# Kernel tuning notes

Hardware: AMD Instinct MI355X
Metric: run time of the kernel (lower is better)

Reference implementation:

```python
import jax, jax.numpy as jnp
import numpy as np

N = 3000          # num_sample (nodes)
N_OMICS = 3000    # input feature dims for both omics
ENC1, ENC2, NZ = 256, 128, 64


def _xavier(key, fan_in, fan_out):
    limit = float(np.sqrt(6.0 / (fan_in + fan_out)))
    return jax.random.uniform(key, (fan_in, fan_out), jnp.float32, -limit, limit)


def setup_inputs() -> dict:
    key = jax.random.key(0)
    ks = jax.random.split(key, 20)
    inp = {
        "omics_1": jax.random.normal(ks[0], (N, N_OMICS), jnp.float32),
        "omics_2": jax.random.normal(ks[1], (N, N_OMICS), jnp.float32),
    }
    # random dense adjacency, row-normalized (as a typical normalized graph operator)
    for i, name in enumerate(["adj_feature_omics1", "adj_feature_omics2",
                              "adj_spatial_omics1", "adj_spatial_omics2"]):
        a = jax.random.uniform(ks[2 + i], (N, N), jnp.float32)
        inp[name] = a / jnp.sum(a, axis=1, keepdims=True)
    # GNNLayer weights for the four GAE encoders (xavier uniform, as in reset_parameters)
    dims = [(N_OMICS, ENC1), (ENC1, ENC2), (ENC2, NZ)]
    kidx = 6
    for enc in ["f1", "f2", "s1", "s2"]:
        for li, (fi, fo) in enumerate(dims, start=1):
            inp[f"w_{enc}_{li}"] = _xavier(ks[kidx], fi, fo)
            kidx += 1
    return inp


def _gae_encoder(x, adj, w1, w2, w3):
    # GNNLayer: support = act(x @ W); out = spmm(adj, support). Dropout is identity (eval).
    z = adj @ jnp.tanh(x @ w1)          # [N, ENC1]
    z = adj @ jnp.tanh(z @ w2)          # [N, ENC2]
    z = adj @ (z @ w3)                  # [N, NZ]  (no activation on layer 3)
    adj_hat = jax.nn.sigmoid(z @ z.T)   # [N, N]
    return z, adj_hat


def reference(omics_1, omics_2,
              adj_feature_omics1, adj_feature_omics2,
              adj_spatial_omics1, adj_spatial_omics2,
              w_f1_1, w_f1_2, w_f1_3,
              w_f2_1, w_f2_2, w_f2_3,
              w_s1_1, w_s1_2, w_s1_3,
              w_s2_1, w_s2_2, w_s2_3):
    _, a1 = _gae_encoder(omics_1, adj_feature_omics1, w_f1_1, w_f1_2, w_f1_3)
    _, a2 = _gae_encoder(omics_2, adj_feature_omics2, w_f2_1, w_f2_2, w_f2_3)
    _, a3 = _gae_encoder(omics_1, adj_spatial_omics1, w_s1_1, w_s1_2, w_s1_3)
    _, a4 = _gae_encoder(omics_2, adj_spatial_omics2, w_s2_1, w_s2_2, w_s2_3)
    # stacked reconstructed adjacencies from the four encoders [4, N, N]
    return jnp.stack([a1, a2, a3, a4], axis=0)
```

## Files before the change

### kernel.cpp

```cpp
#include <hip/hip_runtime.h>
#include <stdint.h>
#include <stddef.h>


typedef __attribute__((ext_vector_type(8))) _Float16 half8;
typedef __attribute__((ext_vector_type(4))) float f32x4;

#define PAD 3072
#define MR  3000
#define SQ_STRIDE ((size_t)PAD * PAD)
#define UPA (PAD * PAD / 8)
#define CAST_BLK 576
#define WT_BLK   128

static __device__ __forceinline__ void async_cp16(const _Float16* g, _Float16* l) {
    __builtin_amdgcn_global_load_lds((const __attribute__((address_space(1))) void*)g,
                                     (__attribute__((address_space(3))) void*)l, 16, 0, 0);
}

struct PrepArgs {
    const float* csrc[2];  _Float16* cdst[2];
    const float* Wsrc[12]; _Float16* Wdst[3];
};

__global__ __launch_bounds__(256) void prep2(PrepArgs p) {
    __shared__ _Float16 lt[64 * 64];
    const int b = blockIdx.x;
    const int t = threadIdx.x;
    if (b < CAST_BLK) {
        const int TOT = 2 * UPA;
        for (int base = b * 2048; base < TOT; base += CAST_BLK * 2048) {
            f32x4 v[8][2];
            #pragma unroll
            for (int k = 0; k < 8; ++k) {
                const int u   = base + (k << 8) + t;
                const int arr = u / UPA;
                const int rem = u - arr * UPA;
                const int row = rem / 384;
                const int c0  = (rem - row * 384) * 8;
                if (row < MR && c0 < MR) {
                    const float* sp = p.csrc[arr] + (size_t)row * MR + c0;
                    v[k][0] = __builtin_nontemporal_load((const f32x4*)sp);
                    v[k][1] = __builtin_nontemporal_load((const f32x4*)(sp + 4));
                } else {
                    v[k][0] = (f32x4){0.f, 0.f, 0.f, 0.f};
                    v[k][1] = (f32x4){0.f, 0.f, 0.f, 0.f};
                }
            }
            #pragma unroll
            for (int k = 0; k < 8; ++k) {
                const int u   = base + (k << 8) + t;
                const int arr = u / UPA;
                const int rem = u - arr * UPA;
                const int row = rem / 384;
                const int c0  = (rem - row * 384) * 8;
                half8 h;
                #pragma unroll
                for (int j = 0; j < 4; ++j) {
                    h[j]     = (_Float16)v[k][0][j];
                    h[4 + j] = (_Float16)v[k][1][j];
                }
                *(half8*)(p.cdst[arr] + (size_t)row * PAD + c0) = h;
            }
        }
    } else {
        for (int tile = b - CAST_BLK; tile < 816; tile += WT_BLK) {
            const int enc = tile / 204;
            int rem = tile - enc * 204;
            const float* src; _Float16* dst; int fi, fo, ldk, kt, rt;
            if (rem < 192) {
                src = p.Wsrc[enc * 3 + 0]; dst = p.Wdst[0] + (size_t)enc * 256 * PAD;
                fi = MR; fo = 256; ldk = PAD; kt = rem >> 2; rt = rem & 3;
            } else if (rem < 200) {
                rem -= 192;
                src = p.Wsrc[enc * 3 + 1]; dst = p.Wdst[1] + (size_t)enc * 128 * 256;
                fi = 256; fo = 128; ldk = 256; kt = rem >> 1; rt = rem & 1;
            } else {
                rem -= 200;
                src = p.Wsrc[enc * 3 + 2]; dst = p.Wdst[2] + (size_t)enc * 128 * 128;
                fi = 128; fo = 64; ldk = 128; kt = rem >> 1; rt = rem & 1;
            }
            const int k0 = kt * 64, r0 = rt * 64;
            __syncthreads();
            {
                const int kr = t >> 2, cc = (t & 3) << 4;
                const int gk = k0 + kr;
                const bool kok = gk < fi;
                #pragma unroll
                for (int j = 0; j < 16; ++j) {
                    const int gr = r0 + cc + j;
                    const float v = (kok && gr < fo) ? src[(size_t)gk * fo + gr] : 0.f;
                    lt[(cc + j) * 64 + kr] = (_Float16)v;
                }
            }
            __syncthreads();
            {
                const int rr = t >> 2, kk = (t & 3) << 4;
                half8 a  = *(half8*)&lt[rr * 64 + kk];
                half8 bb = *(half8*)&lt[rr * 64 + kk + 8];
                _Float16* dp = dst + (size_t)(r0 + rr) * ldk + k0 + kk;
                *(half8*)dp = a;
                *(half8*)(dp + 8) = bb;
            }
        }
    }
}

struct GArgs {
    const _Float16* Aall; size_t aStride; int aMask;
    const _Float16* Ball; size_t bStride; int bMask;
    void* Call; size_t cStride;
    int M, Ncols, Kp, lda, ldb, ldc, mBound, nBound;
};
struct CastA { const float* src[4]; _Float16* dst; };

template<int ACT, int OMODE, int S, int CAST>
__global__ __launch_bounds__(256, 3)
void gemm_bt(GArgs ga, CastA ca)
{
    __shared__ _Float16 smem[16384];

    const int z   = blockIdx.z;
    const int e   = z / S;
    const int ksl = z - e * S;
    const int Kslice = ga.Kp / S;
    const int kbase  = ksl * Kslice;

    const _Float16* A = ga.Aall + (size_t)(e & ga.aMask) * ga.aStride;
    const _Float16* B = ga.Ball + (size_t)(e & ga.bMask) * ga.bStride;

    const int tm = blockIdx.x * 128;
    const int tn = blockIdx.y * 128;
    const int t    = threadIdx.x;
    const int lane = t & 63;
    const int w    = t >> 6;
    const int wm   = (w >> 1) * 64;
    const int wn   = (w & 1) * 64;
    const int lr   = lane & 15;
    const int lg   = lane >> 4;

    const int sr  = t >> 2;
    const int sch = t & 3;

    f32x4 acc[4][4];
    const f32x4 zero = {0.f, 0.f, 0.f, 0.f};
    #pragma unroll
    for (int i = 0; i < 4; ++i)
        #pragma unroll
        for (int j = 0; j < 4; ++j) acc[i][j] = zero;

    const int nht = Kslice >> 5;

    const int fid = blockIdx.x + gridDim.x * (blockIdx.y + gridDim.y * blockIdx.z);
    f32x4 cv0, cv1;
    _Float16* cdp = nullptr;

    auto STAGE = [&](int ht, int buf) {
        const int k0 = kbase + (ht << 5);
        _Float16* As = smem + buf * 8192;
        _Float16* Bs = As + 4096;
        #pragma unroll
        for (int i = 0; i < 2; ++i) {
            const int row = sr + i * 64;
            const int sc  = sch ^ (row & 3);
            async_cp16(A + (size_t)(tm + row) * ga.lda + k0 + sc * 8,
                       As + (row * 4 + sch) * 8);
        }
        #pragma unroll
        for (int i = 0; i < 2; ++i) {
            const int row = sr + i * 64;
            const int sc  = sch ^ (row & 3);
            async_cp16(B + (size_t)(tn + row) * ga.ldb + k0 + sc * 8,
                       Bs + (row * 4 + sch) * 8);
        }
    };

    STAGE(0, 0);
    __syncthreads();
    for (int h = 0; h < nht; ++h) {
        const int cur = h & 1;
        if (h + 1 < nht) STAGE(h + 1, cur ^ 1);
        if (CAST) {
            if (h > 0) {
                half8 hh;
                #pragma unroll
                for (int j = 0; j < 4; ++j) {
                    hh[j] = (_Float16)cv0[j]; hh[4 + j] = (_Float16)cv1[j];
                }
                *(half8*)cdp = hh;
            }
            const int g    = (fid * nht + h) * 256 + t;
            const int arr  = g / UPA;
            const int rem  = g - arr * UPA;
            const int crow = rem / 384;
            const int cc0  = (rem - crow * 384) * 8;
            cdp = ca.dst + (size_t)arr * SQ_STRIDE + (size_t)crow * PAD + cc0;
            if (crow < MR && cc0 < MR) {
                const float* sp = ca.src[arr] + (size_t)crow * MR + cc0;
                cv0 = __builtin_nontemporal_load((const f32x4*)sp);
                cv1 = __builtin_nontemporal_load((const f32x4*)(sp + 4));
            } else {
                cv0 = (f32x4){0.f, 0.f, 0.f, 0.f};
                cv1 = (f32x4){0.f, 0.f, 0.f, 0.f};
            }
        }
        const _Float16* As = smem + cur * 8192;
        const _Float16* Bs = As + 4096;
        half8 af[4], bf[4];
        #pragma unroll
        for (int mi = 0; mi < 4; ++mi) {
            const int ra = wm + mi * 16 + lr;
            const int ch = lg ^ (ra & 3);
            af[mi] = *(const half8*)(As + ra * 32 + ch * 8);
        }
        #pragma unroll
        for (int ni = 0; ni < 4; ++ni) {
            const int rb = wn + ni * 16 + lr;
            const int ch = lg ^ (rb & 3);
            bf[ni] = *(const half8*)(Bs + rb * 32 + ch * 8);
        }
        #pragma unroll
        for (int mi = 0; mi < 4; ++mi)
            #pragma unroll
            for (int ni = 0; ni < 4; ++ni)
                acc[mi][ni] = __builtin_amdgcn_mfma_f32_16x16x32_f16(
                    af[mi], bf[ni], acc[mi][ni], 0, 0, 0);
        __syncthreads();
    }
    if (CAST) {
        half8 hh;
        #pragma unroll
        for (int j = 0; j < 4; ++j) {
            hh[j] = (_Float16)cv0[j]; hh[4 + j] = (_Float16)cv1[j];
        }
        *(half8*)cdp = hh;
    }

    if (OMODE == 0) {
        _Float16* C = (_Float16*)ga.Call + (size_t)e * ga.cStride;
        #pragma unroll
        for (int mi = 0; mi < 4; ++mi)
            #pragma unroll
            for (int rr = 0; rr < 4; ++rr) {
                const int m = tm + wm + mi * 16 + lg * 4 + rr;
                #pragma unroll
                for (int ni = 0; ni < 4; ++ni) {
                    const int n = tn + wn + ni * 16 + lr;
                    float x = acc[mi][ni][rr];
                    if (ACT) x = tanhf(x);
                    const bool ok = (m < ga.M) && (n < ga.Ncols);
                    C[(size_t)m * ga.ldc + n] = ok ? (_Float16)x : (_Float16)0.f;
                }
            }
    } else if (OMODE == 1) {
        _Float16* Cp = (_Float16*)ga.Call + (size_t)z * ga.cStride;
        _Float16* ep = smem + w * 2048;
        #pragma unroll
        for (int hs = 0; hs < 2; ++hs) {
            __syncthreads();
            #pragma unroll
            for (int mi2 = 0; mi2 < 2; ++mi2)
                #pragma unroll
                for (int ni = 0; ni < 4; ++ni)
                    #pragma unroll
                    for (int rr = 0; rr < 4; ++rr) {
                        const int row = mi2 * 16 + lg * 4 + rr;
                        const int col = ni * 16 + lr;
                        const int sw  = (((row ^ (row >> 2)) & 3) << 4);
                        ep[row * 64 + (col ^ sw)] = (_Float16)acc[hs * 2 + mi2][ni][rr];
                    }
            __syncthreads();
            #pragma unroll
            for (int it = 0; it < 4; ++it) {
                const int row = it * 8 + (lane >> 3);
                const int c0  = (lane & 7) * 8;
                const int sw  = (((row ^ (row >> 2)) & 3) << 4);
                half8 v = *(const half8*)&ep[row * 64 + (c0 ^ sw)];
                const int gm = tm + wm + hs * 32 + row;
                const int gn = tn + wn + c0;
                *(half8*)&((_Float16*)Cp)[(size_t)gm * ga.ldc + gn] = v;
            }
        }
    } else {
        float* Cp = (float*)ga.Call + (size_t)e * ga.cStride;
        float* ep = (float*)smem + w * 2048;
        #pragma unroll
        for (int hs = 0; hs < 2; ++hs) {
            __syncthreads();
            #pragma unroll
            for (int mi2 = 0; mi2 < 2; ++mi2)
                #pragma unroll
                for (int ni = 0; ni < 4; ++ni)
                    #pragma unroll
                    for (int rr = 0; rr < 4; ++rr) {
                        const int row = mi2 * 16 + lg * 4 + rr;
                        const int col = ni * 16 + lr;
                        const int sw  = (((row ^ (row >> 2)) & 3) << 4);
                        ep[row * 64 + (col ^ sw)] = acc[hs * 2 + mi2][ni][rr];
                    }
            __syncthreads();
            #pragma unroll
            for (int r2 = 0; r2 < 8; ++r2) {
                const int row = r2 * 4 + (lane >> 4);
                const int c4  = (lane & 15) * 4;
                const int sw  = (((row ^ (row >> 2)) & 3) << 4);
                f32x4 v = *(const f32x4*)&ep[row * 64 + (c4 ^ sw)];
                const int gm = tm + wm + hs * 32 + row;
                const int gn = tn + wn + c4;
                if (gm < ga.mBound && gn < ga.nBound) {
                    #pragma unroll
                    for (int j = 0; j < 4; ++j)
                        v[j] = 1.0f / (1.0f + __expf(-v[j]));
                    __builtin_nontemporal_store(v, (f32x4*)&Cp[(size_t)gm * ga.ldc + gn]);
                }
            }
        }
    }
}

template<int ACT, int S>
__global__ __launch_bounds__(256)
void reduce_k(const _Float16* __restrict__ P, _Float16* __restrict__ out, size_t region)
{
    const size_t e    = blockIdx.y;
    const size_t base = (size_t)(blockIdx.x * 256 + threadIdx.x) * 8;
    const _Float16* p0 = P + e * S * region + base;
    float s[8] = {0.f, 0.f, 0.f, 0.f, 0.f, 0.f, 0.f, 0.f};
    #pragma unroll
    for (int si = 0; si < S; ++si) {
        half8 v = *(const half8*)(p0 + (size_t)si * region);
        #pragma unroll
        for (int j = 0; j < 8; ++j) s[j] += (float)v[j];
    }
    half8 h;
    #pragma unroll
    for (int j = 0; j < 8; ++j) {
        float x = s[j];
        if (ACT) x = tanhf(x);
        h[j] = (_Float16)x;
    }
    *(half8*)(out + e * region + base) = h;
}

extern "C" void kernel_launch(void* const* d_in, const int* in_sizes, int n_in,
                              void* d_out, int out_size, void* d_ws, size_t ws_size,
                              hipStream_t stream)
{
    const size_t R1 = 786432;
    const size_t R2 = 393216;

    _Float16* Adj    = (_Float16*)d_out;
    _Float16* Part16 = Adj + 4 * SQ_STRIDE;

    _Float16* hb = (_Float16*)d_ws;
    size_t off = 0;
    auto alloc = [&](size_t elems) { _Float16* p = hb + off; off += elems; return p; };
    _Float16* Xh  = alloc(2 * SQ_STRIDE);
    _Float16* T1  = alloc(4 * R1);
    _Float16* Z1  = alloc(4 * R1);
    _Float16* T2  = alloc(4 * R2);
    _Float16* Z2  = alloc(4 * R2);
    _Float16* T3  = alloc(4 * R2);
    _Float16* Z3  = alloc(4 * R2);
    _Float16* W1t = alloc(4ull * 256 * PAD);
    _Float16* W2t = alloc(4ull * 128 * 256);
    _Float16* W3t = alloc(4ull * 128 * 128);

    PrepArgs pa;
    pa.csrc[0] = (const float*)d_in[0]; pa.cdst[0] = Xh;
    pa.csrc[1] = (const float*)d_in[1]; pa.cdst[1] = Xh + SQ_STRIDE;
    for (int enc = 0; enc < 4; ++enc)
        for (int li = 0; li < 3; ++li)
            pa.Wsrc[enc * 3 + li] = (const float*)d_in[6 + enc * 3 + li];
    pa.Wdst[0] = W1t; pa.Wdst[1] = W2t; pa.Wdst[2] = W3t;
    prep2<<<dim3(CAST_BLK + WT_BLK, 1, 1), 256, 0, stream>>>(pa);

    const int BIG = 1 << 30;
    CastA cnone = { { nullptr, nullptr, nullptr, nullptr }, nullptr };

    GArgs g1 = { W1t, (size_t)256 * PAD, 3, Xh, SQ_STRIDE, 1,
                 Part16, R1, 256, PAD, PAD, PAD, PAD, PAD, BIG, BIG };
    CastA ca;
    for (int i = 0; i < 4; ++i) ca.src[i] = (const float*)d_in[2 + i];
    ca.dst = Adj;
    gemm_bt<0, 1, 4, 1><<<dim3(2, 24, 16), 256, 0, stream>>>(g1, ca);
    reduce_k<1, 4><<<dim3(384, 4, 1), 256, 0, stream>>>(Part16, T1, R1);

    GArgs g2 = { Adj, SQ_STRIDE, 3, T1, R1, 3,
                 Part16, R1, PAD, 256, PAD, PAD, PAD, 256, BIG, BIG };
    gemm_bt<0, 1, 4, 0><<<dim3(24, 2, 16), 256, 0, stream>>>(g2, cnone);
    reduce_k<0, 4><<<dim3(384, 4, 1), 256, 0, stream>>>(Part16, Z1, R1);

    GArgs g3 = { W2t, (size_t)128 * 256, 3, Z1, R1, 3,
                 T2, R2, 128, PAD, 256, 256, 256, PAD, BIG, BIG };
    gemm_bt<1, 0, 1, 0><<<dim3(1, 24, 4), 256, 0, stream>>>(g3, cnone);

    GArgs g4 = { Adj, SQ_STRIDE, 3, T2, R2, 3,
                 Part16, R2, PAD, 128, PAD, PAD, PAD, 128, BIG, BIG };
    gemm_bt<0, 1, 8, 0><<<dim3(24, 1, 32), 256, 0, stream>>>(g4, cnone);
    reduce_k<0, 8><<<dim3(192, 4, 1), 256, 0, stream>>>(Part16, Z2, R2);

    GArgs g5 = { W3t, (size_t)128 * 128, 3, Z2, R2, 3,
                 T3, R2, 128, PAD, 128, 128, 128, PAD, BIG, BIG };
    gemm_bt<0, 0, 1, 0><<<dim3(1, 24, 4), 256, 0, stream>>>(g5, cnone);

    GArgs g6 = { Adj, SQ_STRIDE, 3, T3, R2, 3,
                 Part16, R2, PAD, 128, PAD, PAD, PAD, 128, BIG, BIG };
    gemm_bt<0, 1, 8, 0><<<dim3(24, 1, 32), 256, 0, stream>>>(g6, cnone);
    reduce_k<0, 8><<<dim3(192, 4, 1), 256, 0, stream>>>(Part16, Z3, R2);

    GArgs g7 = { Z3, R2, 3, Z3, R2, 3,
                 d_out, (size_t)MR * MR, MR, MR, 64, 128, 128, MR, MR, MR };
    gemm_bt<0, 2, 1, 0><<<dim3(24, 24, 4), 256, 0, stream>>>(g7, cnone);
}
```

Before: 258.7 us.

## Exploit symmetry of Z·Zᵀ, deepen split-K, raise occupancy, enlarge cast grid

Z·Zᵀ is symmetric, so the final sigmoid GEMM now computes only the lower-triangle tiles (300 instead of 576 per encoder). Each tile writes its result both directly and, through an LDS transpose, to the mirrored position. Split-K factors for the adjacency GEMMs are doubled to 8 and 16 to expose more parallelism, and the reductions are adjusted to match. Non-cast GEMMs get a launch bound of 4 waves per SIMD, and the cast prep grid is doubled. The risks are extra reduction traffic from the deeper partial sums and register pressure from the higher occupancy target.

New measurement: 326.7 us. 26.3% more time.

```diff
diff --git a/kernel.cpp b/kernel.cpp
--- a/kernel.cpp
+++ b/kernel.cpp
@@ -10,7 +10,7 @@
 #define MR  3000
 #define SQ_STRIDE ((size_t)PAD * PAD)
 #define UPA (PAD * PAD / 8)
-#define CAST_BLK 576
+#define CAST_BLK 1152
 #define WT_BLK   128
 
 static __device__ __forceinline__ void async_cp16(const _Float16* g, _Float16* l) {
@@ -114,8 +114,8 @@
 };
 struct CastA { const float* src[4]; _Float16* dst; };
 
-template<int ACT, int OMODE, int S, int CAST>
-__global__ __launch_bounds__(256, 3)
+template<int ACT, int OMODE, int S, int CAST, int SYM>
+__global__ __launch_bounds__(256, CAST ? 3 : 4)
 void gemm_bt(GArgs ga, CastA ca)
 {
     __shared__ _Float16 smem[16384];
@@ -129,8 +129,16 @@
     const _Float16* A = ga.Aall + (size_t)(e & ga.aMask) * ga.aStride;
     const _Float16* B = ga.Ball + (size_t)(e & ga.bMask) * ga.bStride;
 
-    const int tm = blockIdx.x * 128;
-    const int tn = blockIdx.y * 128;
+    int bx = blockIdx.x, by = blockIdx.y;
+    if (SYM) {
+        const int pp = blockIdx.x;
+        int byy = (int)((__fsqrt_rn(8.f * pp + 1.f) - 1.f) * 0.5f);
+        while ((byy + 1) * (byy + 2) / 2 <= pp) ++byy;
+        while (byy * (byy + 1) / 2 > pp) --byy;
+        by = byy; bx = pp - byy * (byy + 1) / 2;
+    }
+    const int tm = bx * 128;
+    const int tn = by * 128;
     const int t    = threadIdx.x;
     const int lane = t & 63;
     const int w    = t >> 6;
@@ -314,6 +322,37 @@
                     __builtin_nontemporal_store(v, (f32x4*)&Cp[(size_t)gm * ga.ldc + gn]);
                 }
             }
+            if (SYM) {
+                __syncthreads();
+                #pragma unroll
+                for (int mi2 = 0; mi2 < 2; ++mi2)
+                    #pragma unroll
+                    for (int ni = 0; ni < 4; ++ni)
+                        #pragma unroll
+                        for (int rr = 0; rr < 4; ++rr) {
+                            const int row = mi2 * 16 + lg * 4 + rr;
+                            const int col = ni * 16 + lr;
+                            ep[col * 32 + (row ^ ((col & 7) << 2))] =
+                                acc[hs * 2 + mi2][ni][rr];
+                        }
+                __syncthreads();
+                #pragma unroll
+                for (int it = 0; it < 8; ++it) {
+                    const int q  = it * 64 + lane;
+                    const int c  = q >> 3;
+                    const int r4 = (q & 7) * 4;
+                    f32x4 v = *(const f32x4*)&ep[c * 32 + (r4 ^ ((c & 7) << 2))];
+                    const int grow = tn + wn + c;
+                    const int gcol = tm + wm + hs * 32 + r4;
+                    if (grow < ga.mBound && gcol < ga.nBound) {
+                        #pragma unroll
+                        for (int j = 0; j < 4; ++j)
+                            v[j] = 1.0f / (1.0f + __expf(-v[j]));
+                        __builtin_nontemporal_store(
+                            v, (f32x4*)&Cp[(size_t)grow * ga.ldc + gcol]);
+                    }
+                }
+            }
         }
     }
 }
@@ -383,33 +422,33 @@
     CastA ca;
     for (int i = 0; i < 4; ++i) ca.src[i] = (const float*)d_in[2 + i];
     ca.dst = Adj;
-    gemm_bt<0, 1, 4, 1><<<dim3(2, 24, 16), 256, 0, stream>>>(g1, ca);
+    gemm_bt<0, 1, 4, 1, 0><<<dim3(2, 24, 16), 256, 0, stream>>>(g1, ca);
     reduce_k<1, 4><<<dim3(384, 4, 1), 256, 0, stream>>>(Part16, T1, R1);
 
     GArgs g2 = { Adj, SQ_STRIDE, 3, T1, R1, 3,
                  Part16, R1, PAD, 256, PAD, PAD, PAD, 256, BIG, BIG };
-    gemm_bt<0, 1, 4, 0><<<dim3(24, 2, 16), 256, 0, stream>>>(g2, cnone);
-    reduce_k<0, 4><<<dim3(384, 4, 1), 256, 0, stream>>>(Part16, Z1, R1);
+    gemm_bt<0, 1, 8, 0, 0><<<dim3(24, 2, 32), 256, 0, stream>>>(g2, cnone);
+    reduce_k<0, 8><<<dim3(384, 4, 1), 256, 0, stream>>>(Part16, Z1, R1);
 
     GArgs g3 = { W2t, (size_t)128 * 256, 3, Z1, R1, 3,
                  T2, R2, 128, PAD, 256, 256, 256, PAD, BIG, BIG };
-    gemm_bt<1, 0, 1, 0><<<dim3(1, 24, 4), 256, 0, stream>>>(g3, cnone);
+    gemm_bt<1, 0, 1, 0, 0><<<dim3(1, 24, 4), 256, 0, stream>>>(g3, cnone);
 
     GArgs g4 = { Adj, SQ_STRIDE, 3, T2, R2, 3,
                  Part16, R2, PAD, 128, PAD, PAD, PAD, 128, BIG, BIG };
-    gemm_bt<0, 1, 8, 0><<<dim3(24, 1, 32), 256, 0, stream>>>(g4, cnone);
-    reduce_k<0, 8><<<dim3(192, 4, 1), 256, 0, stream>>>(Part16, Z2, R2);
+    gemm_bt<0, 1, 16, 0, 0><<<dim3(24, 1, 64), 256, 0, stream>>>(g4, cnone);
+    reduce_k<0, 16><<<dim3(192, 4, 1), 256, 0, stream>>>(Part16, Z2, R2);
 
     GArgs g5 = { W3t, (size_t)128 * 128, 3, Z2, R2, 3,
                  T3, R2, 128, PAD, 128, 128, 128, PAD, BIG, BIG };
-    gemm_bt<0, 0, 1, 0><<<dim3(1, 24, 4), 256, 0, stream>>>(g5, cnone);
+    gemm_bt<0, 0, 1, 0, 0><<<dim3(1, 24, 4), 256, 0, stream>>>(g5, cnone);
 
     GArgs g6 = { Adj, SQ_STRIDE, 3, T3, R2, 3,
                  Part16, R2, PAD, 128, PAD, PAD, PAD, 128, BIG, BIG };
-    gemm_bt<0, 1, 8, 0><<<dim3(24, 1, 32), 256, 0, stream>>>(g6, cnone);
-    reduce_k<0, 8><<<dim3(192, 4, 1), 256, 0, stream>>>(Part16, Z3, R2);
+    gemm_bt<0, 1, 16, 0, 0><<<dim3(24, 1, 64), 256, 0, stream>>>(g6, cnone);
+    reduce_k<0, 16><<<dim3(192, 4, 1), 256, 0, stream>>>(Part16, Z3, R2);
 
     GArgs g7 = { Z3, R2, 3, Z3, R2, 3,
                  d_out, (size_t)MR * MR, MR, MR, 64, 128, 128, MR, MR, MR };
-    gemm_bt<0, 2, 1, 0><<<dim3(24, 24, 4), 256, 0, stream>>>(g7, cnone);
+    gemm_bt<0, 2, 1, 0, 1><<<dim3(300, 1, 4), 256, 0, stream>>>(g7, cnone);
 }
```
